# Kernel tuning notes

Measured on AMD Instinct MI355X. Metric: run time of the kernel, lower is better.

## Reference

```python
import jax, jax.numpy as jnp
import numpy as np

B, T, S, E = 32, 256, 9, 631     # batch, time, index_len, emb_num
D, FF, H, L, OUT = 512, 512, 8, 2, 512  # d_model, ffn, heads, layers, output_dim
HD = D // H
EPS = 1e-5


def _layernorm(x, g, b):
    m = jnp.mean(x, axis=-1, keepdims=True)
    v = jnp.mean(jnp.square(x - m), axis=-1, keepdims=True)
    return (x - m) * jax.lax.rsqrt(v + EPS) * g + b


def _encoder_layer(h, qkv_w, qkv_b, out_w, out_b, ln1_g, ln1_b,
                   lin1_w, lin1_b, lin2_w, lin2_b, ln2_g, ln2_b):
    # h: (N, S, D). PyTorch post-norm TransformerEncoderLayer, relu activation, dropout=0.
    N = h.shape[0]
    qkv = h @ qkv_w + qkv_b                       # (N, S, 3D)
    q, k, v = jnp.split(qkv, 3, axis=-1)
    q = q.reshape(N, S, H, HD)
    k = k.reshape(N, S, H, HD)
    v = v.reshape(N, S, H, HD)
    scores = jnp.einsum('nqhd,nkhd->nhqk', q, k) / jnp.sqrt(jnp.float32(HD))
    attn = jax.nn.softmax(scores, axis=-1)
    ctx = jnp.einsum('nhqk,nkhd->nqhd', attn, v).reshape(N, S, D)
    h = _layernorm(h + (ctx @ out_w + out_b), ln1_g, ln1_b)
    ff = jax.nn.relu(h @ lin1_w + lin1_b) @ lin2_w + lin2_b
    return _layernorm(h + ff, ln2_g, ln2_b)


def _forward(x, adapt2_w, adapt2_b, adapt_w, adapt_b,
             qkv_w, qkv_b, out_w, out_b, ln1_g, ln1_b,
             lin1_w, lin1_b, lin2_w, lin2_b, ln2_g, ln2_b, fc_w, fc_b):
    # eye_mat[x] @ W^T is a row gather: adapt_layer(onehot) == adapt_w[x] + adapt_b
    emb = adapt_w[x] + adapt_b                               # (B, T, S, D)
    # adapt_ly2(onehot.reshape(B,T,9*E)) == sum_n W2r[n, x[...,n]] + b
    w2r = adapt2_w.reshape(S, E, OUT)
    raw_emb = w2r[jnp.arange(S)[None, None, :], x].sum(axis=2) + adapt2_b  # (B, T, OUT)

    h = emb.reshape(B * T, S, D)
    for l in range(L):
        h = _encoder_layer(h, qkv_w[l], qkv_b[l], out_w[l], out_b[l],
                           ln1_g[l], ln1_b[l], lin1_w[l], lin1_b[l],
                           lin2_w[l], lin2_b[l], ln2_g[l], ln2_b[l])
    cls = h[:, 0, :]                                         # x[0] in seq-first layout
    ov = (cls @ fc_w + fc_b).reshape(B, T, OUT)
    return raw_emb * (1.0 + jax.nn.relu(ov))


def setup_inputs() -> dict:
    key = jax.random.key(0)
    ks = jax.random.split(key, 20)
    s = 0.02
    inp = {
        'x': jax.random.randint(ks[0], (B, T, S), 0, E),
        'adapt2_w': jax.random.normal(ks[1], (S * E, OUT), jnp.float32) * s,
        'adapt2_b': jnp.zeros((OUT,), jnp.float32),
        'adapt_w': jax.random.normal(ks[2], (E, D), jnp.float32) * s,
        'adapt_b': jnp.zeros((D,), jnp.float32),
        'qkv_w': jax.random.normal(ks[3], (L, D, 3 * D), jnp.float32) * s,
        'qkv_b': jnp.zeros((L, 3 * D), jnp.float32),
        'out_w': jax.random.normal(ks[4], (L, D, D), jnp.float32) * s,
        'out_b': jnp.zeros((L, D), jnp.float32),
        'ln1_g': jnp.ones((L, D), jnp.float32),
        'ln1_b': jnp.zeros((L, D), jnp.float32),
        'lin1_w': jax.random.normal(ks[5], (L, D, FF), jnp.float32) * s,
        'lin1_b': jnp.zeros((L, FF), jnp.float32),
        'lin2_w': jax.random.normal(ks[6], (L, FF, D), jnp.float32) * s,
        'lin2_b': jnp.zeros((L, D), jnp.float32),
        'ln2_g': jnp.ones((L, D), jnp.float32),
        'ln2_b': jnp.zeros((L, D), jnp.float32),
        'fc_w': jax.random.normal(ks[7], (D, OUT), jnp.float32) * s,
        'fc_b': jnp.zeros((OUT,), jnp.float32),
    }
    return inp


def reference(x, adapt2_w, adapt2_b, adapt_w, adapt_b, qkv_w, qkv_b, out_w,
              out_b, ln1_g, ln1_b, lin1_w, lin1_b, lin2_w, lin2_b, ln2_g,
              ln2_b, fc_w, fc_b):
    return _forward(x, adapt2_w, adapt2_b, adapt_w, adapt_b, qkv_w, qkv_b,
                    out_w, out_b, ln1_g, ln1_b, lin1_w, lin1_b, lin2_w,
                    lin2_b, ln2_g, ln2_b, fc_w, fc_b)
```

## Files before the change

kernel.cpp:

```cpp
#include <hip/hip_runtime.h>
#include <hip/hip_bf16.h>
#include <stdint.h>

typedef __bf16 bf16;
typedef bf16 bf16x8 __attribute__((ext_vector_type(8)));
typedef float f32x4 __attribute__((ext_vector_type(4)));

__device__ __forceinline__ float b2f(bf16 x) {
  unsigned short u = __builtin_bit_cast(unsigned short, x);
  unsigned int v = ((unsigned int)u) << 16;
  return __builtin_bit_cast(float, v);
}
__device__ __forceinline__ bf16 f2b(float f) {
  unsigned int u = __builtin_bit_cast(unsigned int, f);
  unsigned int r = (u + 0x7FFFu + ((u >> 16) & 1u)) >> 16;
  return __builtin_bit_cast(bf16, (unsigned short)r);
}

__device__ __forceinline__ void async_copy16(const bf16* g, bf16* l) {
  __builtin_amdgcn_global_load_lds(
      (const __attribute__((address_space(1))) void*)g,
      (__attribute__((address_space(3))) void*)l, 16, 0, 0);
}

template <int LDA, int LDC, int RSTR, bool RELU, bool RESID, bool RAWG, bool F32OUT>
__global__ __launch_bounds__(256, 4) void gemm_kernel(
    const bf16* __restrict__ A,
    const bf16* __restrict__ BT,
    const float* __restrict__ bias,
    const bf16* __restrict__ resid,
    const float* __restrict__ rawg,
    bf16* __restrict__ Cb, float* __restrict__ Cf)
{
  constexpr int K = 512;
  __shared__ bf16 As[128 * 64];
  __shared__ bf16 Bs[128 * 64];
  const int t = threadIdx.x;
  const int lane = t & 63;
  const int wave = t >> 6;
  const long m0 = (long)blockIdx.y * 128;
  const int n0 = blockIdx.x * 128;
  const int wm = (wave >> 1) * 64;
  const int wn = (wave & 1) * 64;
  const int row16 = lane & 15;
  const int quad = lane >> 4;

  f32x4 acc[4][4] = {};

  const bf16* gA[4]; const bf16* gB[4];
  bf16* lA[4]; bf16* lB[4];
#pragma unroll
  for (int i = 0; i < 4; i++) {
    int c = i * 256 + t;
    int row = c >> 3;
    int kc = (c & 7) ^ (row & 7);
    gA[i] = A + (m0 + row) * LDA + kc * 8;
    gB[i] = BT + (long)(n0 + row) * K + kc * 8;
    lA[i] = As + i * 2048 + wave * 512;
    lB[i] = Bs + i * 2048 + wave * 512;
  }

  const int rb7 = row16 & 7;
  const bf16* paA = As + (wm + row16) * 64;
  const bf16* pbB = Bs + (wn + row16) * 64;
  const int o0 = ((0 + quad) ^ rb7) * 8;
  const int o1 = ((4 + quad) ^ rb7) * 8;

#pragma unroll 1
  for (int kt = 0; kt < K; kt += 64) {
#pragma unroll
    for (int i = 0; i < 4; i++) async_copy16(gA[i] + kt, lA[i]);
#pragma unroll
    for (int i = 0; i < 4; i++) async_copy16(gB[i] + kt, lB[i]);
    __syncthreads();
    {
      bf16x8 af[4], bfr[4];
#pragma unroll
      for (int i = 0; i < 4; i++) af[i] = *(const bf16x8*)(paA + i * 1024 + o0);
#pragma unroll
      for (int i = 0; i < 4; i++) bfr[i] = *(const bf16x8*)(pbB + i * 1024 + o0);
#pragma unroll
      for (int mi = 0; mi < 4; mi++)
#pragma unroll
        for (int ni = 0; ni < 4; ni++)
          acc[mi][ni] = __builtin_amdgcn_mfma_f32_16x16x32_bf16(af[mi], bfr[ni], acc[mi][ni], 0, 0, 0);
    }
    {
      bf16x8 af[4], bfr[4];
#pragma unroll
      for (int i = 0; i < 4; i++) af[i] = *(const bf16x8*)(paA + i * 1024 + o1);
#pragma unroll
      for (int i = 0; i < 4; i++) bfr[i] = *(const bf16x8*)(pbB + i * 1024 + o1);
#pragma unroll
      for (int mi = 0; mi < 4; mi++)
#pragma unroll
        for (int ni = 0; ni < 4; ni++)
          acc[mi][ni] = __builtin_amdgcn_mfma_f32_16x16x32_bf16(af[mi], bfr[ni], acc[mi][ni], 0, 0, 0);
    }
    __syncthreads();
  }

  float bv[4];
#pragma unroll
  for (int ni = 0; ni < 4; ni++) bv[ni] = bias[n0 + wn + ni * 16 + row16];
#pragma unroll
  for (int mi = 0; mi < 4; mi++) {
    long rb = m0 + wm + mi * 16 + quad * 4;
#pragma unroll
    for (int ni = 0; ni < 4; ni++) {
      int col = n0 + wn + ni * 16 + row16;
#pragma unroll
      for (int r = 0; r < 4; r++) {
        float xv = acc[mi][ni][r] + bv[ni];
        if (RESID) xv += b2f(resid[(rb + r) * RSTR + col]);
        if (RELU) xv = fmaxf(xv, 0.f);
        if (RAWG) xv = rawg[(rb + r) * 512 + col] * (1.f + fmaxf(xv, 0.f));
        if (F32OUT) Cf[(rb + r) * LDC + col] = xv;
        else        Cb[(rb + r) * LDC + col] = f2b(xv);
      }
    }
  }
}

#define APAD 516
__global__ __launch_bounds__(512) void attn_kernel(bf16* __restrict__ qkv)
{
  __shared__ float q[9 * APAD];
  __shared__ float k[9 * APAD];
  __shared__ float v[9 * APAD];
  __shared__ float sc[8 * 81];
  const long n = blockIdx.x;
  const int t = threadIdx.x;
  bf16* base = qkv + n * (9 * 1536);
  for (int c = t; c < 1728; c += 512) {
    int o = c * 8;
    int s = o / 1536;
    int col = o - s * 1536;
    bf16x8 rawv = *(const bf16x8*)(base + o);
    float* dst;
    int cc;
    if (col < 512)       { dst = q; cc = col; }
    else if (col < 1024) { dst = k; cc = col - 512; }
    else                 { dst = v; cc = col - 1024; }
    dst += s * APAD + cc;
#pragma unroll
    for (int j = 0; j < 8; j++) dst[j] = b2f(rawv[j]);
  }
  __syncthreads();
  for (int id = t; id < 648; id += 512) {
    int h = id / 81;
    int r = id - h * 81;
    int si = r / 9;
    int sj = r - si * 9;
    const float* qp = q + si * APAD + h * 64;
    const float* kp = k + sj * APAD + h * 64;
    float acc = 0.f;
#pragma unroll
    for (int j = 0; j < 64; j += 4) {
      float4 qa = *(const float4*)(qp + j);
      float4 ka = *(const float4*)(kp + j);
      acc += qa.x * ka.x + qa.y * ka.y + qa.z * ka.z + qa.w * ka.w;
    }
    sc[h * 81 + si * 9 + sj] = acc * 0.125f;
  }
  __syncthreads();
  if (t < 72) {
    int h = t / 9, si = t - h * 9;
    float* row = sc + h * 81 + si * 9;
    float m = row[0];
    for (int j = 1; j < 9; j++) m = fmaxf(m, row[j]);
    float s = 0.f;
    float e[9];
    for (int j = 0; j < 9; j++) { e[j] = __expf(row[j] - m); s += e[j]; }
    float inv = 1.f / s;
    for (int j = 0; j < 9; j++) row[j] = e[j] * inv;
  }
  __syncthreads();
  for (int e = t; e < 4608; e += 512) {
    int si = e >> 9;
    int c = e & 511;
    int h = c >> 6;
    const float* ar = sc + h * 81 + si * 9;
    float acc = 0.f;
#pragma unroll
    for (int sj = 0; sj < 9; sj++) acc += ar[sj] * v[sj * APAD + c];
    base[si * 1536 + c] = f2b(acc);
  }
}

__global__ __launch_bounds__(256) void ln_kernel(const bf16* __restrict__ in, long istride,
                                                 const float* __restrict__ g, const float* __restrict__ b,
                                                 bf16* __restrict__ out, long ostride)
{
  const int t = threadIdx.x;
  const int lane = t & 63;
  const int wave = t >> 6;
  const long row = (long)blockIdx.x * 4 + wave;
  const bf16* p = in + row * istride + lane * 8;
  bf16x8 xv = *(const bf16x8*)p;
  float x[8];
  float s = 0.f;
#pragma unroll
  for (int j = 0; j < 8; j++) { x[j] = b2f(xv[j]); s += x[j]; }
#pragma unroll
  for (int off = 32; off; off >>= 1) s += __shfl_xor(s, off);
  float mean = s * (1.f / 512.f);
  float vv = 0.f;
#pragma unroll
  for (int j = 0; j < 8; j++) { float d = x[j] - mean; vv += d * d; }
#pragma unroll
  for (int off = 32; off; off >>= 1) vv += __shfl_xor(vv, off);
  float inv = rsqrtf(vv * (1.f / 512.f) + 1e-5f);
  float4 g0 = *(const float4*)(g + lane * 8);
  float4 g1 = *(const float4*)(g + lane * 8 + 4);
  float4 b0 = *(const float4*)(b + lane * 8);
  float4 b1 = *(const float4*)(b + lane * 8 + 4);
  float gg[8] = {g0.x, g0.y, g0.z, g0.w, g1.x, g1.y, g1.z, g1.w};
  float bb[8] = {b0.x, b0.y, b0.z, b0.w, b1.x, b1.y, b1.z, b1.w};
  bf16x8 o;
#pragma unroll
  for (int j = 0; j < 8; j++) o[j] = f2b((x[j] - mean) * inv * gg[j] + bb[j]);
  *(bf16x8*)(out + row * ostride + lane * 8) = o;
}

__global__ __launch_bounds__(256) void emb_kernel(const int* __restrict__ x, const float* __restrict__ aw,
                                                  const float* __restrict__ ab, bf16* __restrict__ h)
{
  const int t = threadIdx.x;
  const int lane = t & 63;
  const long row = (long)blockIdx.x * 4 + (t >> 6);
  const int ix = x[row];
  const float* w = aw + (long)ix * 512 + lane * 8;
  float4 w0 = *(const float4*)(w);
  float4 w1 = *(const float4*)(w + 4);
  float4 a0 = *(const float4*)(ab + lane * 8);
  float4 a1 = *(const float4*)(ab + lane * 8 + 4);
  float ww[8] = {w0.x, w0.y, w0.z, w0.w, w1.x, w1.y, w1.z, w1.w};
  float aa[8] = {a0.x, a0.y, a0.z, a0.w, a1.x, a1.y, a1.z, a1.w};
  bf16x8 o;
#pragma unroll
  for (int j = 0; j < 8; j++) o[j] = f2b(ww[j] + aa[j]);
  *(bf16x8*)(h + row * 512 + lane * 8) = o;
}

__global__ __launch_bounds__(256) void rawemb_kernel(const int* __restrict__ x, const float* __restrict__ w2,
                                                     const float* __restrict__ b2, float* __restrict__ raw)
{
  const long n = blockIdx.x;
  const int t = threadIdx.x;
  const int c = t * 2;
  float a0 = b2[c], a1 = b2[c + 1];
  for (int s = 0; s < 9; s++) {
    int ix = x[n * 9 + s];
    const float* p = w2 + ((long)(s * 631 + ix)) * 512 + c;
    a0 += p[0];
    a1 += p[1];
  }
  raw[n * 512 + c] = a0;
  raw[n * 512 + c + 1] = a1;
}

struct TP { const float* src[9]; bf16* dst[9]; int n[9]; };
__global__ __launch_bounds__(256) void transpose_kernel(TP p)
{
  const int mid = blockIdx.z;
  const int N = p.n[mid];
  if ((int)blockIdx.x * 32 >= N) return;
  const float* src = p.src[mid];
  bf16* dst = p.dst[mid];
  __shared__ float tile[32][33];
  const int tx = threadIdx.x & 31;
  const int ty0 = (threadIdx.x >> 5) * 4;
  const long kb = (long)blockIdx.y * 32, nb = (long)blockIdx.x * 32;
#pragma unroll
  for (int i = 0; i < 4; i++) tile[ty0 + i][tx] = src[(kb + ty0 + i) * N + nb + tx];
  __syncthreads();
#pragma unroll
  for (int i = 0; i < 4; i++) dst[(nb + ty0 + i) * 512 + kb + tx] = f2b(tile[tx][ty0 + i]);
}

extern "C" void kernel_launch(void* const* d_in, const int* in_sizes, int n_in,
                              void* d_out, int out_size, void* d_ws, size_t ws_size,
                              hipStream_t stream)
{
  (void)in_sizes; (void)n_in; (void)out_size;
  const int*   x        = (const int*)d_in[0];
  const float* adapt2_w = (const float*)d_in[1];
  const float* adapt2_b = (const float*)d_in[2];
  const float* adapt_w  = (const float*)d_in[3];
  const float* adapt_b  = (const float*)d_in[4];
  const float* qkv_w    = (const float*)d_in[5];
  const float* qkv_b    = (const float*)d_in[6];
  const float* out_w    = (const float*)d_in[7];
  const float* out_b    = (const float*)d_in[8];
  const float* ln1_g    = (const float*)d_in[9];
  const float* ln1_b    = (const float*)d_in[10];
  const float* lin1_w   = (const float*)d_in[11];
  const float* lin1_b   = (const float*)d_in[12];
  const float* lin2_w   = (const float*)d_in[13];
  const float* lin2_b   = (const float*)d_in[14];
  const float* ln2_g    = (const float*)d_in[15];
  const float* ln2_b    = (const float*)d_in[16];
  const float* fc_w     = (const float*)d_in[17];
  const float* fc_b     = (const float*)d_in[18];
  float* outp = (float*)d_out;
  char* ws = (char*)d_ws;

  const long wTbytes = 6815744L;
  int G = 64;
  const int cand[7] = {1, 2, 4, 8, 16, 32, 64};
  for (int i = 0; i < 7; i++) {
    long rows = 73728L / cand[i], seqs = 8192L / cand[i];
    long need = wTbytes + rows * 1024 + rows * 3072 + seqs * 2048;
    if (need <= (long)ws_size) { G = cand[i]; break; }
  }
  const long rows_c = 73728L / G;
  const long seqs_c = 8192L / G;

  bf16*  wT    = (bf16*)(ws);
  bf16*  h_c   = (bf16*)(ws + wTbytes);
  bf16*  Qc    = (bf16*)(ws + wTbytes + rows_c * 1024);
  float* raw_c = (float*)(ws + wTbytes + rows_c * 1024 + rows_c * 3072);
  bf16* qkvT  = wT;
  bf16* outT  = wT + 1572864;
  bf16* lin1T = wT + 2097152;
  bf16* lin2T = wT + 2621440;
  bf16* fcT   = wT + 3145728;

  TP tp;
  tp.src[0] = qkv_w;           tp.dst[0] = qkvT;           tp.n[0] = 1536;
  tp.src[1] = qkv_w + 786432;  tp.dst[1] = qkvT + 786432;  tp.n[1] = 1536;
  tp.src[2] = out_w;           tp.dst[2] = outT;           tp.n[2] = 512;
  tp.src[3] = out_w + 262144;  tp.dst[3] = outT + 262144;  tp.n[3] = 512;
  tp.src[4] = lin1_w;          tp.dst[4] = lin1T;          tp.n[4] = 512;
  tp.src[5] = lin1_w + 262144; tp.dst[5] = lin1T + 262144; tp.n[5] = 512;
  tp.src[6] = lin2_w;          tp.dst[6] = lin2T;          tp.n[6] = 512;
  tp.src[7] = lin2_w + 262144; tp.dst[7] = lin2T + 262144; tp.n[7] = 512;
  tp.src[8] = fc_w;            tp.dst[8] = fcT;            tp.n[8] = 512;
  hipLaunchKernelGGL(transpose_kernel, dim3(48, 16, 9), dim3(256), 0, stream, tp);

  const bf16*  nullb = nullptr;
  const float* nullf = nullptr;
  float*       nullfo = nullptr;

  for (int g = 0; g < G; g++) {
    const long row0 = (long)g * rows_c;
    const long seq0 = (long)g * seqs_c;

    hipLaunchKernelGGL(emb_kernel, dim3(rows_c / 4), dim3(256), 0, stream,
        x + row0, adapt_w, adapt_b, h_c);
    hipLaunchKernelGGL(rawemb_kernel, dim3(seqs_c), dim3(256), 0, stream,
        x + seq0 * 9, adapt2_w, adapt2_b, raw_c);

    for (int l = 0; l < 2; l++) {
      hipLaunchKernelGGL((gemm_kernel<512, 1536, 1, false, false, false, false>),
          dim3(12, rows_c / 128), dim3(256), 0, stream,
          h_c, qkvT + l * 786432, qkv_b + l * 1536, nullb, nullf, Qc, nullfo);
      hipLaunchKernelGGL(attn_kernel, dim3(seqs_c), dim3(512), 0, stream, Qc);
      hipLaunchKernelGGL((gemm_kernel<1536, 1536, 512, false, true, false, false>),
          dim3(4, rows_c / 128), dim3(256), 0, stream,
          Qc, outT + l * 262144, out_b + l * 512, h_c, nullf, Qc + 1024, nullfo);
      hipLaunchKernelGGL(ln_kernel, dim3(rows_c / 4), dim3(256), 0, stream,
          Qc + 1024, 1536L, ln1_g + l * 512, ln1_b + l * 512, Qc + 512, 1536L);
      hipLaunchKernelGGL((gemm_kernel<1536, 1536, 1, true, false, false, false>),
          dim3(4, rows_c / 128), dim3(256), 0, stream,
          Qc + 512, lin1T + l * 262144, lin1_b + l * 512, nullb, nullf, Qc, nullfo);
      hipLaunchKernelGGL((gemm_kernel<1536, 512, 1536, false, true, false, false>),
          dim3(4, rows_c / 128), dim3(256), 0, stream,
          Qc, lin2T + l * 262144, lin2_b + l * 512, Qc + 512, nullf, h_c, nullfo);
      hipLaunchKernelGGL(ln_kernel, dim3(rows_c / 4), dim3(256), 0, stream,
          h_c, 512L, ln2_g + l * 512, ln2_b + l * 512, h_c, 512L);
    }

    hipLaunchKernelGGL((gemm_kernel<4608, 512, 1, false, false, true, true>),
        dim3(4, seqs_c / 128), dim3(256), 0, stream,
        h_c, fcT, fc_b, nullb, raw_c, (bf16*)nullptr, outp + seq0 * 512);
  }
}
```

Before: 1.237 ms.

## Enlarge GEMM M-tile to 192 rows and add grouped block swizzle

The GEMM kernel gets a template parameter for the number of 16-row M fragments per wave, and the encoder GEMMs now use 192x128 tiles (6 fragments) instead of 128x128. This raises MFMA work per LDS load and per B-tile fetch, at the cost of more registers, so launch bounds drop to 3 blocks per CU. A block-index swizzle also groups 8 M-tiles per column sweep so that weight tiles and activation rows stay in L2 longer. The risks are lower occupancy and tail effects if rows_c is not a multiple of 192.

New measurement: 1.040 ms. 15.9% less time.

```diff
diff --git a/kernel.cpp b/kernel.cpp
--- a/kernel.cpp
+++ b/kernel.cpp
@@ -23,8 +23,8 @@
       (__attribute__((address_space(3))) void*)l, 16, 0, 0);
 }
 
-template <int LDA, int LDC, int RSTR, bool RELU, bool RESID, bool RAWG, bool F32OUT>
-__global__ __launch_bounds__(256, 4) void gemm_kernel(
+template <int MFR, int LDA, int LDC, int RSTR, bool RELU, bool RESID, bool RAWG, bool F32OUT, bool SWZ>
+__global__ __launch_bounds__(256, (MFR == 6 ? 3 : 4)) void gemm_kernel(
     const bf16* __restrict__ A,
     const bf16* __restrict__ BT,
     const float* __restrict__ bias,
@@ -33,30 +33,58 @@
     bf16* __restrict__ Cb, float* __restrict__ Cf)
 {
   constexpr int K = 512;
-  __shared__ bf16 As[128 * 64];
+  constexpr int MROWS = MFR * 32;
+  __shared__ bf16 As[MROWS * 64];
   __shared__ bf16 Bs[128 * 64];
   const int t = threadIdx.x;
   const int lane = t & 63;
   const int wave = t >> 6;
-  const long m0 = (long)blockIdx.y * 128;
-  const int n0 = blockIdx.x * 128;
-  const int wm = (wave >> 1) * 64;
+
+  int bx, by;
+  if (SWZ) {
+    const int gn = gridDim.x, gm = gridDim.y;
+    int id = blockIdx.y * gn + blockIdx.x;
+    int full = (gm & ~7) * gn;
+    if (id < full) {
+      int sg = id / (8 * gn);
+      int r = id - sg * (8 * gn);
+      by = sg * 8 + (r & 7);
+      bx = r >> 3;
+    } else {
+      int r = id - full;
+      int rem = gm - (gm & ~7);
+      by = (gm & ~7) + (r % rem);
+      bx = r / rem;
+    }
+  } else {
+    bx = blockIdx.x; by = blockIdx.y;
+  }
+
+  const long m0 = (long)by * MROWS;
+  const int n0 = bx * 128;
+  const int wm = (wave >> 1) * (MFR * 16);
   const int wn = (wave & 1) * 64;
   const int row16 = lane & 15;
   const int quad = lane >> 4;
 
-  f32x4 acc[4][4] = {};
-
-  const bf16* gA[4]; const bf16* gB[4];
-  bf16* lA[4]; bf16* lB[4];
+  f32x4 acc[MFR][4] = {};
+
+  const bf16* gA[MFR]; const bf16* gB[4];
+  bf16* lA[MFR]; bf16* lB[4];
+#pragma unroll
+  for (int i = 0; i < MFR; i++) {
+    int c = i * 256 + t;
+    int row = c >> 3;
+    int kc = (c & 7) ^ (row & 7);
+    gA[i] = A + (m0 + row) * LDA + kc * 8;
+    lA[i] = As + i * 2048 + wave * 512;
+  }
 #pragma unroll
   for (int i = 0; i < 4; i++) {
     int c = i * 256 + t;
     int row = c >> 3;
     int kc = (c & 7) ^ (row & 7);
-    gA[i] = A + (m0 + row) * LDA + kc * 8;
     gB[i] = BT + (long)(n0 + row) * K + kc * 8;
-    lA[i] = As + i * 2048 + wave * 512;
     lB[i] = Bs + i * 2048 + wave * 512;
   }
 
@@ -69,30 +97,30 @@
 #pragma unroll 1
   for (int kt = 0; kt < K; kt += 64) {
 #pragma unroll
-    for (int i = 0; i < 4; i++) async_copy16(gA[i] + kt, lA[i]);
+    for (int i = 0; i < MFR; i++) async_copy16(gA[i] + kt, lA[i]);
 #pragma unroll
     for (int i = 0; i < 4; i++) async_copy16(gB[i] + kt, lB[i]);
     __syncthreads();
     {
-      bf16x8 af[4], bfr[4];
-#pragma unroll
-      for (int i = 0; i < 4; i++) af[i] = *(const bf16x8*)(paA + i * 1024 + o0);
+      bf16x8 af[MFR], bfr[4];
+#pragma unroll
+      for (int i = 0; i < MFR; i++) af[i] = *(const bf16x8*)(paA + i * 1024 + o0);
 #pragma unroll
       for (int i = 0; i < 4; i++) bfr[i] = *(const bf16x8*)(pbB + i * 1024 + o0);
 #pragma unroll
-      for (int mi = 0; mi < 4; mi++)
+      for (int mi = 0; mi < MFR; mi++)
 #pragma unroll
         for (int ni = 0; ni < 4; ni++)
           acc[mi][ni] = __builtin_amdgcn_mfma_f32_16x16x32_bf16(af[mi], bfr[ni], acc[mi][ni], 0, 0, 0);
     }
     {
-      bf16x8 af[4], bfr[4];
-#pragma unroll
-      for (int i = 0; i < 4; i++) af[i] = *(const bf16x8*)(paA + i * 1024 + o1);
+      bf16x8 af[MFR], bfr[4];
+#pragma unroll
+      for (int i = 0; i < MFR; i++) af[i] = *(const bf16x8*)(paA + i * 1024 + o1);
 #pragma unroll
       for (int i = 0; i < 4; i++) bfr[i] = *(const bf16x8*)(pbB + i * 1024 + o1);
 #pragma unroll
-      for (int mi = 0; mi < 4; mi++)
+      for (int mi = 0; mi < MFR; mi++)
 #pragma unroll
         for (int ni = 0; ni < 4; ni++)
           acc[mi][ni] = __builtin_amdgcn_mfma_f32_16x16x32_bf16(af[mi], bfr[ni], acc[mi][ni], 0, 0, 0);
@@ -104,7 +132,7 @@
 #pragma unroll
   for (int ni = 0; ni < 4; ni++) bv[ni] = bias[n0 + wn + ni * 16 + row16];
 #pragma unroll
-  for (int mi = 0; mi < 4; mi++) {
+  for (int mi = 0; mi < MFR; mi++) {
     long rb = m0 + wm + mi * 16 + quad * 4;
 #pragma unroll
     for (int ni = 0; ni < 4; ni++) {
@@ -353,26 +381,26 @@
         x + seq0 * 9, adapt2_w, adapt2_b, raw_c);
 
     for (int l = 0; l < 2; l++) {
-      hipLaunchKernelGGL((gemm_kernel<512, 1536, 1, false, false, false, false>),
-          dim3(12, rows_c / 128), dim3(256), 0, stream,
+      hipLaunchKernelGGL((gemm_kernel<6, 512, 1536, 1, false, false, false, false, true>),
+          dim3(12, rows_c / 192), dim3(256), 0, stream,
           h_c, qkvT + l * 786432, qkv_b + l * 1536, nullb, nullf, Qc, nullfo);
       hipLaunchKernelGGL(attn_kernel, dim3(seqs_c), dim3(512), 0, stream, Qc);
-      hipLaunchKernelGGL((gemm_kernel<1536, 1536, 512, false, true, false, false>),
-          dim3(4, rows_c / 128), dim3(256), 0, stream,
+      hipLaunchKernelGGL((gemm_kernel<6, 1536, 1536, 512, false, true, false, false, true>),
+          dim3(4, rows_c / 192), dim3(256), 0, stream,
           Qc, outT + l * 262144, out_b + l * 512, h_c, nullf, Qc + 1024, nullfo);
       hipLaunchKernelGGL(ln_kernel, dim3(rows_c / 4), dim3(256), 0, stream,
           Qc + 1024, 1536L, ln1_g + l * 512, ln1_b + l * 512, Qc + 512, 1536L);
-      hipLaunchKernelGGL((gemm_kernel<1536, 1536, 1, true, false, false, false>),
-          dim3(4, rows_c / 128), dim3(256), 0, stream,
+      hipLaunchKernelGGL((gemm_kernel<6, 1536, 1536, 1, true, false, false, false, true>),
+          dim3(4, rows_c / 192), dim3(256), 0, stream,
           Qc + 512, lin1T + l * 262144, lin1_b + l * 512, nullb, nullf, Qc, nullfo);
-      hipLaunchKernelGGL((gemm_kernel<1536, 512, 1536, false, true, false, false>),
-          dim3(4, rows_c / 128), dim3(256), 0, stream,
+      hipLaunchKernelGGL((gemm_kernel<6, 1536, 512, 1536, false, true, false, false, true>),
+          dim3(4, rows_c / 192), dim3(256), 0, stream,
           Qc, lin2T + l * 262144, lin2_b + l * 512, Qc + 512, nullf, h_c, nullfo);
       hipLaunchKernelGGL(ln_kernel, dim3(rows_c / 4), dim3(256), 0, stream,
           h_c, 512L, ln2_g + l * 512, ln2_b + l * 512, h_c, 512L);
     }
 
-    hipLaunchKernelGGL((gemm_kernel<4608, 512, 1, false, false, true, true>),
+    hipLaunchKernelGGL((gemm_kernel<4, 4608, 512, 1, false, false, true, true, false>),
         dim3(4, seqs_c / 128), dim3(256), 0, stream,
         h_c, fcT, fc_b, nullb, raw_c, (bf16*)nullptr, outp + seq0 * 512);
   }
```
